# Optimization experiments

Hardware: AMD Instinct MI355X
Metric: run time of the kernel (lower is better)

The kernel has to match this reference:

```python
import jax, jax.numpy as jnp
import numpy as np

N0, N1, N2, N3, B = 120000, 20000, 6000, 1600, 64
E1, E2, E3 = 480000, 144000, 38400
KS = 5  # kernel size per dim; K = 125 total


def spline_basis(pseudo, ks=KS):
    # open B-spline basis, degree 1, over [0,1]^3 (torch_spline_conv semantics)
    p = pseudo * (ks - 1)                       # (E,3)
    lo = jnp.clip(jnp.floor(p), 0.0, ks - 2.0)  # (E,3)
    f = p - lo                                  # fractional part
    bits = jnp.array([[(s >> d) & 1 for d in range(3)] for s in range(8)],
                     dtype=jnp.float32)         # (8,3) corner offsets
    w = jnp.where(bits[None] > 0, f[:, None, :], 1.0 - f[:, None, :])  # (E,8,3)
    basis = w[..., 0] * w[..., 1] * w[..., 2]   # (E,8)
    strides = jnp.array([1.0, ks, ks * ks], dtype=jnp.float32)
    kidx = ((lo[:, None, :] + bits[None]) * strides).sum(-1).astype(jnp.int32)  # (E,8)
    return basis, kidx


def spline_conv(x, edge_index, pseudo, W, root, bias, num_nodes):
    src, dst = edge_index[0], edge_index[1]
    basis, kidx = spline_basis(pseudo)                   # (E,8), (E,8)
    XW = jnp.einsum('ni,kio->nko', x, W)                 # (N,K,out)
    taps = XW[src[:, None], kidx]                        # (E,8,out) gather
    msg = (taps * basis[..., None]).sum(axis=1)          # (E,out)
    agg = jax.ops.segment_sum(msg, dst, num_segments=num_nodes)
    deg = jax.ops.segment_sum(jnp.ones_like(dst, jnp.float32), dst,
                              num_segments=num_nodes)
    agg = agg / jnp.maximum(deg, 1.0)[:, None]           # mean aggregation
    return agg + x @ root + bias


def seg_max(x, seg, n):
    v = jax.ops.segment_max(x, seg, num_segments=n)
    return jnp.where(jnp.isfinite(v), v, 0.0)  # empty voxels -> 0


def setup_inputs() -> dict:
    key = jax.random.key(0)
    ks = jax.random.split(key, 24)
    return {
        'x0': jax.random.uniform(ks[0], (N0, 1), jnp.float32),
        'cluster0': jax.random.randint(ks[1], (N0,), 0, N1),
        'edge1': jax.random.randint(ks[2], (2, E1), 0, N1),
        'pseudo1': jax.random.uniform(ks[3], (E1, 3), jnp.float32),
        'W1': jax.random.normal(ks[4], (125, 1, 64), jnp.float32) * 0.1,
        'root1': jax.random.normal(ks[5], (1, 64), jnp.float32) * 0.1,
        'b1': jnp.zeros((64,), jnp.float32),
        'cluster1': jax.random.randint(ks[6], (N1,), 0, N2),
        'edge2': jax.random.randint(ks[7], (2, E2), 0, N2),
        'pseudo2': jax.random.uniform(ks[8], (E2, 3), jnp.float32),
        'W2': jax.random.normal(ks[9], (125, 64, 64), jnp.float32) * 0.05,
        'root2': jax.random.normal(ks[10], (64, 64), jnp.float32) * 0.05,
        'b2': jnp.zeros((64,), jnp.float32),
        'cluster2': jax.random.randint(ks[11], (N2,), 0, N3),
        'edge3': jax.random.randint(ks[12], (2, E3), 0, N3),
        'pseudo3': jax.random.uniform(ks[13], (E3, 3), jnp.float32),
        'W3': jax.random.normal(ks[14], (125, 64, 128), jnp.float32) * 0.05,
        'root3': jax.random.normal(ks[15], (64, 128), jnp.float32) * 0.05,
        'b3': jnp.zeros((128,), jnp.float32),
        'cluster3': jax.random.randint(ks[16], (N3,), 0, B * 8),
        'fc1_w': jax.random.normal(ks[17], (1024, 256), jnp.float32) * 0.03,
        'fc1_b': jnp.zeros((256,), jnp.float32),
        'fc2_w': jax.random.normal(ks[18], (256, 10), jnp.float32) * 0.06,
        'fc2_b': jnp.zeros((10,), jnp.float32),
    }


def reference(x0, cluster0, edge1, pseudo1, W1, root1, b1,
              cluster1, edge2, pseudo2, W2, root2, b2,
              cluster2, edge3, pseudo3, W3, root3, b3,
              cluster3, fc1_w, fc1_b, fc2_w, fc2_b):
    x = seg_max(x0, cluster0, N1)                       # sparse voxel max pool 1
    x = jax.nn.elu(spline_conv(x, edge1, pseudo1, W1, root1, b1, N1))
    x = seg_max(x, cluster1, N2)                        # pool 2
    x = jax.nn.elu(spline_conv(x, edge2, pseudo2, W2, root2, b2, N2))
    x = seg_max(x, cluster2, N3)                        # pool 3
    x = jax.nn.elu(spline_conv(x, edge3, pseudo3, W3, root3, b3, N3))
    x = seg_max(x, cluster3, B * 8)                     # dense 2x2x2 voxel pool
    x = x.reshape(B, 8 * 128)
    x = jax.nn.elu(x @ fc1_w + fc1_b)
    x = x @ fc2_w + fc2_b
    return jax.nn.log_softmax(x, axis=1)
```

## Files before the change

### kernel.cpp

```cpp
#include <hip/hip_runtime.h>
#include <hip/hip_bf16.h>
#include <math.h>

#define N0c 120000
#define N1c 20000
#define N2c 6000
#define N3c 1600
#define E1c 480000
#define E2c 144000
#define E3c 38400

#define HB1 32
#define HB2 120
#define HB3 40
#define CVT2B 2000
#define CVT3B 4000
#define SS0B  469

typedef __attribute__((ext_vector_type(8))) short short8;
typedef __attribute__((ext_vector_type(4))) float f32x4;

__device__ __forceinline__ float eluf(float x) {
    return x > 0.0f ? x : expm1f(x);
}

__device__ __forceinline__ unsigned f2sort(float f) {
    unsigned u = __float_as_uint(f);
    return (u & 0x80000000u) ? ~u : (u | 0x80000000u);
}
__device__ __forceinline__ float sort2f(unsigned u) {
    unsigned bits = (u & 0x80000000u) ? (u & 0x7FFFFFFFu) : ~u;
    return __uint_as_float(bits);
}
__device__ __forceinline__ unsigned short f2bf(float v) {
    unsigned u = __float_as_uint(v);
    unsigned r = (u + 0x7FFFu + ((u >> 16) & 1u)) >> 16;
    return (unsigned short)r;
}

__global__ __launch_bounds__(256) void hist_all(
    const int* __restrict__ edge1, const int* __restrict__ edge2,
    const int* __restrict__ edge3,
    const float* __restrict__ pseudo2, const float* __restrict__ pseudo3,
    const float* __restrict__ W2, const float* __restrict__ W3,
    const float* __restrict__ x0, const int* __restrict__ cluster0,
    int* __restrict__ blockCnt1,
    int* __restrict__ blockCnt2, int* __restrict__ cntD2,
    int* __restrict__ blockCnt3, int* __restrict__ cntD3,
    unsigned short* __restrict__ W2t, unsigned short* __restrict__ W3t,
    unsigned* __restrict__ xm1)
{
    __shared__ int h[1250];
    int b = blockIdx.x, t = threadIdx.x;
    if (b < HB1) {
        for (int i = t; i < 1250; i += 256) h[i] = 0;
        __syncthreads();
        for (int e = b * 256 + t; e < E1c; e += HB1 * 256)
            atomicAdd(&h[edge1[E1c + e] >> 4], 1);
        __syncthreads();
        for (int i = t; i < 1250; i += 256) blockCnt1[i * HB1 + b] = h[i];
    } else if (b < HB1 + HB2 + HB3) {
        bool is2 = b < HB1 + HB2;
        int rb = is2 ? (b - HB1) : (b - HB1 - HB2);
        int nblk = is2 ? HB2 : HB3;
        int E = is2 ? E2c : E3c;
        const int* edge = is2 ? edge2 : edge3;
        const float* pseudo = is2 ? pseudo2 : pseudo3;
        int* blockCnt = is2 ? blockCnt2 : blockCnt3;
        int* dstCnt = is2 ? cntD2 : cntD3;
        int nb = is2 ? HB2 : HB3;
        if (t < 64) h[t] = 0;
        __syncthreads();
        for (int e = rb * 256 + t; e < E; e += nblk * 256) {
            int c = 0, mul = 1;
            #pragma unroll
            for (int d = 0; d < 3; d++) {
                float p = pseudo[e * 3 + d] * 4.0f;
                float l = fminf(fmaxf(floorf(p), 0.0f), 3.0f);
                c += (int)l * mul;
                mul <<= 2;
            }
            atomicAdd(&h[c], 1);
            atomicAdd(&dstCnt[edge[E + e]], 1);
        }
        __syncthreads();
        if (t < 64) blockCnt[t * nb + rb] = h[t];
    } else if (b < HB1 + HB2 + HB3 + CVT2B) {
        int idx = (b - (HB1 + HB2 + HB3)) * 256 + t;
        if (idx < 125 * 64 * 64) {
            int ic = idx & 63, kn = idx >> 6;
            int n = kn & 63, k = kn >> 6;
            W2t[idx] = f2bf(W2[((size_t)k * 64 + ic) * 64 + n]);
        }
    } else if (b < HB1 + HB2 + HB3 + CVT2B + CVT3B) {
        int idx = (b - (HB1 + HB2 + HB3 + CVT2B)) * 256 + t;
        if (idx < 125 * 128 * 64) {
            int ic = idx & 63, kn = idx >> 6;
            int n = kn & 127, k = kn >> 7;
            W3t[idx] = f2bf(W3[((size_t)k * 64 + ic) * 128 + n]);
        }
    } else {
        int idx = (b - (HB1 + HB2 + HB3 + CVT2B + CVT3B)) * 256 + t;
        if (idx < N0c)
            atomicMax(&xm1[cluster0[idx]], f2sort(x0[idx]));
    }
}

__global__ __launch_bounds__(256) void plan_tot(
    const int* __restrict__ blockCnt1, int* __restrict__ start1,
    const int* __restrict__ blockCnt2, int* __restrict__ binCnt2,
    int* __restrict__ binStart2, int* __restrict__ blkPrefix2,
    int* __restrict__ chunkBin2, int* __restrict__ chunkOff2,
    const int* __restrict__ blockCnt3, int* __restrict__ binCnt3,
    int* __restrict__ binStart3, int* __restrict__ blkPrefix3,
    int* __restrict__ chunkBin3, int* __restrict__ chunkOff3)
{
    __shared__ int ps[256];
    __shared__ int ps64[64];
    int t = threadIdx.x;

    int loc[5];
    int s = 0;
    #pragma unroll
    for (int i = 0; i < 5; i++) {
        int bin = t * 5 + i;
        int v = 0;
        if (bin < 1250) {
            const int4* row = (const int4*)(blockCnt1 + (size_t)bin * HB1);
            #pragma unroll
            for (int j = 0; j < HB1 / 4; j++) {
                int4 q = row[j];
                v += q.x + q.y + q.z + q.w;
            }
        }
        loc[i] = v;
        s += v;
    }
    ps[t] = s;
    __syncthreads();
    for (int ofs = 1; ofs < 256; ofs <<= 1) {
        int add = (t >= ofs) ? ps[t - ofs] : 0;
        __syncthreads();
        ps[t] += add;
        __syncthreads();
    }
    int run = (t == 0) ? 0 : ps[t - 1];
    #pragma unroll
    for (int i = 0; i < 5; i++) {
        int bin = t * 5 + i;
        if (bin < 1250) {
            start1[bin] = run;
            run += loc[i];
        }
    }
    if (t == 255) start1[1250] = run;
    __syncthreads();

    if (t < 64) {
        int v = 0;
        const int4* row = (const int4*)(blockCnt2 + (size_t)t * HB2);
        for (int j = 0; j < HB2 / 4; j++) {
            int4 q = row[j];
            v += q.x + q.y + q.z + q.w;
        }
        binCnt2[t] = v;
        ps64[t] = v;
    }
    __syncthreads();
    if (t == 0) {
        int s2 = 0, p = 0;
        for (int c = 0; c < 64; c++) {
            int v = ps64[c];
            binStart2[c] = s2;
            blkPrefix2[c] = p;
            s2 += v;
            p += (v + 63) >> 6;
        }
        binStart2[64] = s2;
        blkPrefix2[64] = p;
    }
    __syncthreads();
    if (t < 64) {
        int nch = (binCnt2[t] + 63) >> 6;
        int base = blkPrefix2[t];
        for (int j = 0; j < nch; j++) {
            chunkBin2[base + j] = t;
            chunkOff2[base + j] = j;
        }
    }
    __syncthreads();

    if (t < 64) {
        int v = 0;
        const int4* row = (const int4*)(blockCnt3 + (size_t)t * HB3);
        for (int j = 0; j < HB3 / 4; j++) {
            int4 q = row[j];
            v += q.x + q.y + q.z + q.w;
        }
        binCnt3[t] = v;
        ps64[t] = v;
    }
    __syncthreads();
    if (t == 0) {
        int s3 = 0, p = 0;
        for (int c = 0; c < 64; c++) {
            int v = ps64[c];
            binStart3[c] = s3;
            blkPrefix3[c] = p;
            s3 += v;
            p += (v + 63) >> 6;
        }
        binStart3[64] = s3;
        blkPrefix3[64] = p;
    }
    __syncthreads();
    if (t < 64) {
        int nch = (binCnt3[t] + 63) >> 6;
        int base = blkPrefix3[t];
        for (int j = 0; j < nch; j++) {
            chunkBin3[base + j] = t;
            chunkOff3[base + j] = j;
        }
    }
}

__global__ __launch_bounds__(256) void off_all(
    const int* __restrict__ blockCnt1, const int* __restrict__ start1,
    int* __restrict__ blockOff1,
    const int* __restrict__ blockCnt2, const int* __restrict__ binStart2,
    int* __restrict__ blockOff2,
    const int* __restrict__ blockCnt3, const int* __restrict__ binStart3,
    int* __restrict__ blockOff3)
{
    int r = blockIdx.x * 256 + threadIdx.x;
    if (r < 1250) {
        int run = start1[r];
        const int* c = blockCnt1 + (size_t)r * HB1;
        int* o = blockOff1 + (size_t)r * HB1;
        #pragma unroll 4
        for (int b = 0; b < HB1; b++) { o[b] = run; run += c[b]; }
    } else if (r < 1250 + 64) {
        int bin = r - 1250;
        int run = binStart2[bin];
        const int* c = blockCnt2 + (size_t)bin * HB2;
        int* o = blockOff2 + (size_t)bin * HB2;
        #pragma unroll 4
        for (int b = 0; b < HB2; b++) { o[b] = run; run += c[b]; }
    } else if (r < 1250 + 128) {
        int bin = r - 1314;
        int run = binStart3[bin];
        const int* c = blockCnt3 + (size_t)bin * HB3;
        int* o = blockOff3 + (size_t)bin * HB3;
        #pragma unroll 4
        for (int b = 0; b < HB3; b++) { o[b] = run; run += c[b]; }
    }
}

__global__ __launch_bounds__(256) void scatter_all(
    const int* __restrict__ edge1, const float* __restrict__ pseudo1,
    const int* __restrict__ edge2, const float* __restrict__ pseudo2,
    const int* __restrict__ edge3, const float* __restrict__ pseudo3,
    const int* __restrict__ blockOff1, const int* __restrict__ blockOff2,
    const int* __restrict__ blockOff3,
    int4* __restrict__ rec1, int4* __restrict__ rec2, int4* __restrict__ rec3,
    unsigned* __restrict__ xm1)
{
    __shared__ int cur[1250];
    int b = blockIdx.x, t = threadIdx.x;
    if (b < HB1) {
        for (int i = t; i < 1250; i += 256) cur[i] = blockOff1[(size_t)i * HB1 + b];
        __syncthreads();
        for (int e = b * 256 + t; e < E1c; e += HB1 * 256) {
            int src = edge1[e], dst = edge1[E1c + e];
            float f[3];
            int kbase = 0, mul5 = 1;
            #pragma unroll
            for (int d = 0; d < 3; d++) {
                float pp = pseudo1[e * 3 + d] * 4.0f;
                float l = fminf(fmaxf(floorf(pp), 0.0f), 3.0f);
                f[d] = pp - l;
                kbase += (int)l * mul5;
                mul5 *= 5;
            }
            int p = atomicAdd(&cur[dst >> 4], 1);
            rec1[p] = make_int4(src | ((dst & 15) << 16) | (kbase << 20),
                                __float_as_int(f[0]), __float_as_int(f[1]),
                                __float_as_int(f[2]));
        }
    } else if (b < HB1 + HB2 + HB3) {
        bool is2 = b < HB1 + HB2;
        int rb = is2 ? (b - HB1) : (b - HB1 - HB2);
        int nblk = is2 ? HB2 : HB3;
        int E = is2 ? E2c : E3c;
        const int* edge = is2 ? edge2 : edge3;
        const float* pseudo = is2 ? pseudo2 : pseudo3;
        const int* blockOff = is2 ? blockOff2 : blockOff3;
        int4* rec = is2 ? rec2 : rec3;
        int nb = is2 ? HB2 : HB3;
        if (t < 64) cur[t] = blockOff[(size_t)t * nb + rb];
        __syncthreads();
        for (int e = rb * 256 + t; e < E; e += nblk * 256) {
            int src = edge[e], dst = edge[E + e];
            float f[3];
            int c = 0, mul = 1;
            #pragma unroll
            for (int d = 0; d < 3; d++) {
                float pp = pseudo[e * 3 + d] * 4.0f;
                float l = fminf(fmaxf(floorf(pp), 0.0f), 3.0f);
                f[d] = pp - l;
                c += (int)l * mul;
                mul <<= 2;
            }
            int p = atomicAdd(&cur[c], 1);
            rec[p] = make_int4(src | (dst << 16),
                               __float_as_int(f[0]), __float_as_int(f[1]),
                               __float_as_int(f[2]));
        }
    } else {
        int idx = (b - (HB1 + HB2 + HB3)) * 256 + t;
        if (idx < N1c) {
            float f = sort2f(xm1[idx]);
            unsigned bb = __float_as_uint(f);
            if ((bb & 0x7F800000u) == 0x7F800000u) f = 0.0f;
            ((float*)xm1)[idx] = f;
        }
    }
}

__global__ __launch_bounds__(256) void conv1_block(
    const int4* __restrict__ rec, const float* __restrict__ x,
    const int* __restrict__ start,
    const float* __restrict__ W, const float* __restrict__ root,
    const float* __restrict__ bias, const int* __restrict__ cl,
    unsigned* __restrict__ xmOut) {
    __shared__ float T[16][128];
    __shared__ int degL[16];
    int b = blockIdx.x;
    for (int j = threadIdx.x; j < 2048; j += 256) ((float*)T)[j] = 0.0f;
    if (threadIdx.x < 16) degL[threadIdx.x] = 0;
    __syncthreads();
    int s0 = start[b], s1 = start[b + 1];
    for (int i = s0 + threadIdx.x; i < s1; i += 256) {
        int4 r = rec[i];
        int src = r.x & 0xFFFF;
        int ln = (r.x >> 16) & 15;
        int kbase = r.x >> 20;
        float f0 = __int_as_float(r.y);
        float f1 = __int_as_float(r.z);
        float f2 = __int_as_float(r.w);
        float xv = x[src];
        #pragma unroll
        for (int s = 0; s < 8; s++) {
            int b0 = s & 1, b1 = (s >> 1) & 1, b2 = (s >> 2) & 1;
            float w0 = b0 ? f0 : 1.0f - f0;
            float w1 = b1 ? f1 : 1.0f - f1;
            float w2 = b2 ? f2 : 1.0f - f2;
            int k = kbase + b0 + 5 * b1 + 25 * b2;
            atomicAdd(&T[ln][k], xv * w0 * w1 * w2);
        }
        atomicAdd(&degL[ln], 1);
    }
    __syncthreads();
    int w = threadIdx.x >> 6, lane = threadIdx.x & 63;
    float acc[4] = {0.0f, 0.0f, 0.0f, 0.0f};
    for (int k = 0; k < 125; k++) {
        float wv = W[(k << 6) + lane];
        #pragma unroll
        for (int j = 0; j < 4; j++)
            acc[j] = fmaf(T[w + 4 * j][k], wv, acc[j]);
    }
    int v0 = b << 4;
    #pragma unroll
    for (int j = 0; j < 4; j++) {
        int ln = w + 4 * j;
        int v = v0 + ln;
        float d = fmaxf((float)degL[ln], 1.0f);
        float val = eluf(acc[j] / d + x[v] * root[lane] + bias[lane]);
        atomicMax(&xmOut[((size_t)cl[v] << 6) + lane], f2sort(val));
    }
}

__global__ void decode_cvt(unsigned* __restrict__ buf,
                           unsigned short* __restrict__ xb, int total) {
    int idx = blockIdx.x * blockDim.x + threadIdx.x;
    if (idx >= total) return;
    float f = sort2f(buf[idx]);
    unsigned b = __float_as_uint(f);
    if ((b & 0x7F800000u) == 0x7F800000u) f = 0.0f;
    ((float*)buf)[idx] = f;
    xb[idx] = f2bf(f);
}

__global__ void segmax_decode(unsigned* __restrict__ buf, int total) {
    int idx = blockIdx.x * blockDim.x + threadIdx.x;
    if (idx >= total) return;
    float f = sort2f(buf[idx]);
    unsigned b = __float_as_uint(f);
    if ((b & 0x7F800000u) == 0x7F800000u) f = 0.0f;
    ((float*)buf)[idx] = f;
}

template<int COUT>
__global__ __launch_bounds__(256) void spline_mfma(
    const int4* __restrict__ recs,
    const unsigned short* __restrict__ Wt,
    const unsigned short* __restrict__ xb,
    const int* __restrict__ binStart,
    const int* __restrict__ binCnt,
    const int* __restrict__ blkPrefix,
    const int* __restrict__ chunkBin,
    const int* __restrict__ chunkOff,
    float* __restrict__ agg)
{
    __shared__ float basisS[4][8][64];
    __shared__ int srcS[4][64];
    __shared__ int dstS[4][64];

    int w = threadIdx.x >> 6, lane = threadIdx.x & 63;
    int c = blockIdx.x * 4 + w;
    if (c >= blkPrefix[64]) return;
    int bin = chunkBin[c];
    int chunk = chunkOff[c];
    int cnt = binCnt[bin];

    {
        int pos = chunk * 64 + lane;
        bool act = pos < cnt;
        int4 r = act ? recs[binStart[bin] + pos] : make_int4(0, 0, 0, 0);
        srcS[w][lane] = r.x & 0xFFFF;
        dstS[w][lane] = act ? (r.x >> 16) : -1;
        float f0 = __int_as_float(r.y);
        float f1 = __int_as_float(r.z);
        float f2 = __int_as_float(r.w);
        #pragma unroll
        for (int s = 0; s < 8; s++) {
            float w0 = (s & 1) ? f0 : 1.0f - f0;
            float w1 = (s & 2) ? f1 : 1.0f - f1;
            float w2 = (s & 4) ? f2 : 1.0f - f2;
            basisS[w][s][lane] = act ? (w0 * w1 * w2) : 0.0f;
        }
    }
    __builtin_amdgcn_wave_barrier();
    __threadfence_block();

    int lo0 = bin & 3, lo1 = (bin >> 2) & 3, lo2 = bin >> 4;
    int kbase = lo0 + 5 * lo1 + 25 * lo2;
    int colOff = (COUT == 128) ? (blockIdx.y << 6) : 0;
    int q = lane >> 4;
    int mcol = lane & 15;

    short8 afr[4][2];
    #pragma unroll
    for (int rt = 0; rt < 4; rt++) {
        int src = srcS[w][rt * 16 + mcol];
        const unsigned short* xr = xb + ((size_t)src << 6) + q * 8;
        afr[rt][0] = *(const short8*)(xr);
        afr[rt][1] = *(const short8*)(xr + 32);
    }

    f32x4 acc[4][4];
    #pragma unroll
    for (int rt = 0; rt < 4; rt++)
        #pragma unroll
        for (int nt = 0; nt < 4; nt++)
            acc[rt][nt] = (f32x4){0.0f, 0.0f, 0.0f, 0.0f};
    const f32x4 zero4 = {0.0f, 0.0f, 0.0f, 0.0f};

    #pragma unroll 1
    for (int s = 0; s < 8; s++) {
        int k = kbase + (s & 1) + 5 * ((s >> 1) & 1) + 25 * (s >> 2);
        const unsigned short* Wk = Wt + ((size_t)k * COUT + colOff) * 64;
        short8 bfr[4][2];
        #pragma unroll
        for (int nt = 0; nt < 4; nt++) {
            const unsigned short* Wn = Wk + (size_t)(nt * 16 + mcol) * 64 + q * 8;
            bfr[nt][0] = *(const short8*)(Wn);
            bfr[nt][1] = *(const short8*)(Wn + 32);
        }
        #pragma unroll
        for (int rt = 0; rt < 4; rt++) {
            f32x4 ct[4];
            #pragma unroll
            for (int nt = 0; nt < 4; nt++) {
                ct[nt] = __builtin_amdgcn_mfma_f32_16x16x32_bf16(afr[rt][0], bfr[nt][0], zero4, 0, 0, 0);
                ct[nt] = __builtin_amdgcn_mfma_f32_16x16x32_bf16(afr[rt][1], bfr[nt][1], ct[nt], 0, 0, 0);
            }
            #pragma unroll
            for (int r = 0; r < 4; r++) {
                float bs = basisS[w][s][rt * 16 + q * 4 + r];
                #pragma unroll
                for (int nt = 0; nt < 4; nt++)
                    acc[rt][nt][r] = fmaf(bs, ct[nt][r], acc[rt][nt][r]);
            }
        }
    }

    #pragma unroll
    for (int rt = 0; rt < 4; rt++) {
        #pragma unroll
        for (int r = 0; r < 4; r++) {
            int d = dstS[w][rt * 16 + q * 4 + r];
            if (d >= 0) {
                float* ap = agg + (size_t)d * COUT + colOff + mcol;
                #pragma unroll
                for (int nt = 0; nt < 4; nt++)
                    atomicAdd(ap + nt * 16, acc[rt][nt][r]);
            }
        }
    }
}

__global__ __launch_bounds__(256) void node_update64(
    const float* __restrict__ agg, const int* __restrict__ deg,
    const float* __restrict__ xm, const float* __restrict__ root,
    const float* __restrict__ bias, const int* __restrict__ cl,
    unsigned* __restrict__ xmOut, int nNodes) {
    __shared__ float xsh[4][64];
    int w = threadIdx.x >> 6, lane = threadIdx.x & 63;
    int v = blockIdx.x * 4 + w;
    if (v >= nNodes) return;
    xsh[w][lane] = xm[((size_t)v << 6) + lane];
    float a = agg[((size_t)v << 6) + lane] / fmaxf((float)deg[v], 1.0f);
    float r = 0.0f;
    #pragma unroll 8
    for (int i = 0; i < 64; i++)
        r = fmaf(xsh[w][i], root[(i << 6) + lane], r);
    float val = eluf(a + r + bias[lane]);
    atomicMax(&xmOut[((size_t)cl[v] << 6) + lane], f2sort(val));
}

__global__ __launch_bounds__(256) void node_update128(
    const float* __restrict__ agg, const int* __restrict__ deg,
    const float* __restrict__ xm, const float* __restrict__ root,
    const float* __restrict__ bias, const int* __restrict__ cl,
    unsigned* __restrict__ xmOut, int nNodes) {
    __shared__ float xsh[4][64];
    int w = threadIdx.x >> 6, lane = threadIdx.x & 63;
    int v = blockIdx.x * 4 + w;
    if (v >= nNodes) return;
    xsh[w][lane] = xm[((size_t)v << 6) + lane];
    float dinv = 1.0f / fmaxf((float)deg[v], 1.0f);
    float a0 = agg[((size_t)v << 7) + lane] * dinv;
    float a1 = agg[((size_t)v << 7) + 64 + lane] * dinv;
    float r0 = 0.0f, r1 = 0.0f;
    #pragma unroll 8
    for (int i = 0; i < 64; i++) {
        float xi = xsh[w][i];
        r0 = fmaf(xi, root[(i << 7) + lane], r0);
        r1 = fmaf(xi, root[(i << 7) + 64 + lane], r1);
    }
    unsigned* orow = xmOut + ((size_t)cl[v] << 7);
    atomicMax(&orow[lane], f2sort(eluf(a0 + r0 + bias[lane])));
    atomicMax(&orow[64 + lane], f2sort(eluf(a1 + r1 + bias[lane + 64])));
}

__global__ __launch_bounds__(256) void fc1_split(
    const float* __restrict__ xin, const float* __restrict__ w1,
    float* __restrict__ h) {
    __shared__ float xsh[128];
    int row = blockIdx.x, ks = blockIdx.y;
    int o = threadIdx.x;
    if (o < 128) xsh[o] = xin[row * 1024 + ks * 128 + o];
    __syncthreads();
    float acc = 0.0f;
    const float* wp = w1 + (size_t)ks * 128 * 256 + o;
    #pragma unroll 8
    for (int i = 0; i < 128; i++)
        acc = fmaf(xsh[i], wp[i * 256], acc);
    atomicAdd(&h[row * 256 + o], acc);
}

__global__ __launch_bounds__(64) void fc2_k(
    const float* __restrict__ h, const float* __restrict__ b1,
    const float* __restrict__ w2, const float* __restrict__ b2,
    float* __restrict__ out) {
    __shared__ float hs[256];
    __shared__ float lg[10];
    int row = blockIdx.x;
    int t = threadIdx.x;
    for (int i = t; i < 256; i += 64) hs[i] = eluf(h[row * 256 + i] + b1[i]);
    __syncthreads();
    if (t < 10) {
        float a = b2[t];
        for (int i = 0; i < 256; i++) a = fmaf(hs[i], w2[i * 10 + t], a);
        lg[t] = a;
    }
    __syncthreads();
    if (t < 10) {
        float m = -1e30f;
        #pragma unroll
        for (int j = 0; j < 10; j++) m = fmaxf(m, lg[j]);
        float sum = 0.0f;
        #pragma unroll
        for (int j = 0; j < 10; j++) sum += expf(lg[j] - m);
        out[row * 10 + t] = lg[t] - m - logf(sum);
    }
}

extern "C" void kernel_launch(void* const* d_in, const int* in_sizes, int n_in,
                              void* d_out, int out_size, void* d_ws, size_t ws_size,
                              hipStream_t stream) {
    const float* x0      = (const float*)d_in[0];
    const int*   cluster0= (const int*)d_in[1];
    const int*   edge1   = (const int*)d_in[2];
    const float* pseudo1 = (const float*)d_in[3];
    const float* W1      = (const float*)d_in[4];
    const float* root1   = (const float*)d_in[5];
    const float* b1      = (const float*)d_in[6];
    const int*   cluster1= (const int*)d_in[7];
    const int*   edge2   = (const int*)d_in[8];
    const float* pseudo2 = (const float*)d_in[9];
    const float* W2      = (const float*)d_in[10];
    const float* root2   = (const float*)d_in[11];
    const float* b2      = (const float*)d_in[12];
    const int*   cluster2= (const int*)d_in[13];
    const int*   edge3   = (const int*)d_in[14];
    const float* pseudo3 = (const float*)d_in[15];
    const float* W3      = (const float*)d_in[16];
    const float* root3   = (const float*)d_in[17];
    const float* b3      = (const float*)d_in[18];
    const int*   cluster3= (const int*)d_in[19];
    const float* fc1_w   = (const float*)d_in[20];
    const float* fc1_b   = (const float*)d_in[21];
    const float* fc2_w   = (const float*)d_in[22];
    const float* fc2_b   = (const float*)d_in[23];
    float* out = (float*)d_out;

    float* ws = (float*)d_ws;
    size_t off = 0;
    float* xm1  = ws + off; off += 20480;
    float* xm2  = ws + off; off += (size_t)N2c * 64;
    float* xm3  = ws + off; off += (size_t)N3c * 64;
    float* xm4  = ws + off; off += 512 * 128;
    float* agg2 = ws + off; off += (size_t)N2c * 64;
    float* agg3 = ws + off; off += (size_t)N3c * 128;
    float* h1   = ws + off; off += 64 * 256;
    int* cntD2   = (int*)(ws + off); off += 6016;
    int* cntD3   = (int*)(ws + off); off += 1664;
    size_t zeroFloats = off;
    int4* rec1 = (int4*)(ws + off); off += (size_t)E1c * 4;
    int4* rec2 = (int4*)(ws + off); off += (size_t)E2c * 4;
    int4* rec3 = (int4*)(ws + off); off += (size_t)E3c * 4;
    unsigned short* W2t = (unsigned short*)(ws + off); off += 256000;
    unsigned short* W3t = (unsigned short*)(ws + off); off += 512000;
    unsigned short* xb2 = (unsigned short*)(ws + off); off += 192000;
    unsigned short* xb3 = (unsigned short*)(ws + off); off += 51200;
    int* start1    = (int*)(ws + off); off += 1280;
    int* blockCnt1 = (int*)(ws + off); off += HB1 * 1250;
    int* blockOff1 = (int*)(ws + off); off += HB1 * 1250;
    int* blockCnt2 = (int*)(ws + off); off += HB2 * 64;
    int* blockOff2 = (int*)(ws + off); off += HB2 * 64;
    int* blockCnt3 = (int*)(ws + off); off += HB3 * 64;
    int* blockOff3 = (int*)(ws + off); off += HB3 * 64;
    int* binCnt2   = (int*)(ws + off); off += 64;
    int* binStart2 = (int*)(ws + off); off += 80;
    int* blkPrefix2= (int*)(ws + off); off += 80;
    int* chunkBin2 = (int*)(ws + off); off += 2560;
    int* chunkOff2 = (int*)(ws + off); off += 2560;
    int* binCnt3   = (int*)(ws + off); off += 64;
    int* binStart3 = (int*)(ws + off); off += 80;
    int* blkPrefix3= (int*)(ws + off); off += 80;
    int* chunkBin3 = (int*)(ws + off); off += 768;
    int* chunkOff3 = (int*)(ws + off); off += 768;

    hipMemsetAsync(d_ws, 0, zeroFloats * sizeof(float), stream);

    hist_all<<<HB1 + HB2 + HB3 + CVT2B + CVT3B + SS0B, 256, 0, stream>>>(
        edge1, edge2, edge3, pseudo2, pseudo3, W2, W3, x0, cluster0,
        blockCnt1, blockCnt2, cntD2, blockCnt3, cntD3,
        W2t, W3t, (unsigned*)xm1);

    plan_tot<<<1, 256, 0, stream>>>(
        blockCnt1, start1,
        blockCnt2, binCnt2, binStart2, blkPrefix2, chunkBin2, chunkOff2,
        blockCnt3, binCnt3, binStart3, blkPrefix3, chunkBin3, chunkOff3);

    off_all<<<6, 256, 0, stream>>>(
        blockCnt1, start1, blockOff1,
        blockCnt2, binStart2, blockOff2,
        blockCnt3, binStart3, blockOff3);

    scatter_all<<<HB1 + HB2 + HB3 + (N1c + 255) / 256, 256, 0, stream>>>(
        edge1, pseudo1, edge2, pseudo2, edge3, pseudo3,
        blockOff1, blockOff2, blockOff3, rec1, rec2, rec3, (unsigned*)xm1);

    conv1_block<<<1250, 256, 0, stream>>>(rec1, xm1, start1, W1, root1, b1,
                                          cluster1, (unsigned*)xm2);
    decode_cvt<<<(N2c * 64) / 256, 256, 0, stream>>>((unsigned*)xm2, xb2, N2c * 64);

    spline_mfma<64><<<dim3((E2c / 64 + 64 + 3) / 4, 1), 256, 0, stream>>>(
        rec2, W2t, xb2, binStart2, binCnt2, blkPrefix2, chunkBin2, chunkOff2, agg2);
    node_update64<<<(N2c + 3) / 4, 256, 0, stream>>>(agg2, cntD2, xm2, root2, b2,
                                                     cluster2, (unsigned*)xm3, N2c);
    decode_cvt<<<(N3c * 64) / 256, 256, 0, stream>>>((unsigned*)xm3, xb3, N3c * 64);

    spline_mfma<128><<<dim3((E3c / 64 + 64 + 3) / 4, 2), 256, 0, stream>>>(
        rec3, W3t, xb3, binStart3, binCnt3, blkPrefix3, chunkBin3, chunkOff3, agg3);
    node_update128<<<(N3c + 3) / 4, 256, 0, stream>>>(agg3, cntD3, xm3, root3, b3,
                                                      cluster3, (unsigned*)xm4, N3c);
    segmax_decode<<<(512 * 128) / 256, 256, 0, stream>>>((unsigned*)xm4, 512 * 128);

    fc1_split<<<dim3(64, 8), 256, 0, stream>>>(xm4, fc1_w, h1);
    fc2_k<<<64, 64, 0, stream>>>(h1, fc1_b, fc2_w, fc2_b, out);
}
```

Before: 347.4 us.

## Tile weight transpose via LDS, fuse planning kernels, split MFMA columns wider

Weight transpose-and-convert now works one kernel tap per block through a padded LDS tile, giving coalesced reads and packed bf16 pair writes, with far fewer blocks. The offset kernel is merged into the single-block planning kernel, and the segmax decode is folded into fc1's input load, which removes two launches. The spline MFMA kernel now covers 32 output columns per block instead of 64, doubling grid.y for more parallelism and fewer accumulator registers. In exchange, the A fragments and basis are loaded again for each column slice, and more atomic traffic goes to the aggregation buffer.

```diff
diff --git a/kernel.cpp b/kernel.cpp
--- a/kernel.cpp
+++ b/kernel.cpp
@@ -13,9 +13,9 @@
 #define HB1 32
 #define HB2 120
 #define HB3 40
-#define CVT2B 2000
-#define CVT3B 4000
-#define SS0B  469
+#define WT2B 125
+#define WT3B 250
+#define SS0B 469
 
 typedef __attribute__((ext_vector_type(8))) short short8;
 typedef __attribute__((ext_vector_type(4))) float f32x4;
@@ -50,9 +50,10 @@
     unsigned short* __restrict__ W2t, unsigned short* __restrict__ W3t,
     unsigned* __restrict__ xm1)
 {
-    __shared__ int h[1250];
+    __shared__ float tile[64][65];
     int b = blockIdx.x, t = threadIdx.x;
     if (b < HB1) {
+        int* h = (int*)tile;
         for (int i = t; i < 1250; i += 256) h[i] = 0;
         __syncthreads();
         for (int e = b * 256 + t; e < E1c; e += HB1 * 256)
@@ -60,6 +61,7 @@
         __syncthreads();
         for (int i = t; i < 1250; i += 256) blockCnt1[i * HB1 + b] = h[i];
     } else if (b < HB1 + HB2 + HB3) {
+        int* h = (int*)tile;
         bool is2 = b < HB1 + HB2;
         int rb = is2 ? (b - HB1) : (b - HB1 - HB2);
         int nblk = is2 ? HB2 : HB3;
@@ -68,7 +70,6 @@
         const float* pseudo = is2 ? pseudo2 : pseudo3;
         int* blockCnt = is2 ? blockCnt2 : blockCnt3;
         int* dstCnt = is2 ? cntD2 : cntD3;
-        int nb = is2 ? HB2 : HB3;
         if (t < 64) h[t] = 0;
         __syncthreads();
         for (int e = rb * 256 + t; e < E; e += nblk * 256) {
@@ -84,36 +85,60 @@
             atomicAdd(&dstCnt[edge[E + e]], 1);
         }
         __syncthreads();
-        if (t < 64) blockCnt[t * nb + rb] = h[t];
-    } else if (b < HB1 + HB2 + HB3 + CVT2B) {
-        int idx = (b - (HB1 + HB2 + HB3)) * 256 + t;
-        if (idx < 125 * 64 * 64) {
-            int ic = idx & 63, kn = idx >> 6;
-            int n = kn & 63, k = kn >> 6;
-            W2t[idx] = f2bf(W2[((size_t)k * 64 + ic) * 64 + n]);
-        }
-    } else if (b < HB1 + HB2 + HB3 + CVT2B + CVT3B) {
-        int idx = (b - (HB1 + HB2 + HB3 + CVT2B)) * 256 + t;
-        if (idx < 125 * 128 * 64) {
-            int ic = idx & 63, kn = idx >> 6;
-            int n = kn & 127, k = kn >> 7;
-            W3t[idx] = f2bf(W3[((size_t)k * 64 + ic) * 128 + n]);
+        if (t < 64) blockCnt[t * nblk + rb] = h[t];
+    } else if (b < HB1 + HB2 + HB3 + WT2B) {
+        int k = b - (HB1 + HB2 + HB3);
+        int col = t & 63, rq = t >> 6;
+        #pragma unroll
+        for (int i = 0; i < 16; i++) {
+            int ic = i * 4 + rq;
+            tile[ic][col] = W2[((size_t)k * 64 + ic) * 64 + col];
+        }
+        __syncthreads();
+        int n = t >> 2, icq = (t & 3) * 16;
+        unsigned* dst = (unsigned*)(W2t + ((size_t)k * 64 + n) * 64 + icq);
+        #pragma unroll
+        for (int j = 0; j < 8; j++) {
+            unsigned lo = f2bf(tile[icq + 2 * j][n]);
+            unsigned hi = f2bf(tile[icq + 2 * j + 1][n]);
+            dst[j] = lo | (hi << 16);
+        }
+    } else if (b < HB1 + HB2 + HB3 + WT2B + WT3B) {
+        int b2 = b - (HB1 + HB2 + HB3 + WT2B);
+        int k = b2 >> 1, half = (b2 & 1) * 64;
+        int col = t & 63, rq = t >> 6;
+        #pragma unroll
+        for (int i = 0; i < 16; i++) {
+            int ic = i * 4 + rq;
+            tile[ic][col] = W3[((size_t)k * 64 + ic) * 128 + half + col];
+        }
+        __syncthreads();
+        int n = t >> 2, icq = (t & 3) * 16;
+        unsigned* dst = (unsigned*)(W3t + ((size_t)k * 128 + half + n) * 64 + icq);
+        #pragma unroll
+        for (int j = 0; j < 8; j++) {
+            unsigned lo = f2bf(tile[icq + 2 * j][n]);
+            unsigned hi = f2bf(tile[icq + 2 * j + 1][n]);
+            dst[j] = lo | (hi << 16);
         }
     } else {
-        int idx = (b - (HB1 + HB2 + HB3 + CVT2B + CVT3B)) * 256 + t;
+        int idx = (b - (HB1 + HB2 + HB3 + WT2B + WT3B)) * 256 + t;
         if (idx < N0c)
             atomicMax(&xm1[cluster0[idx]], f2sort(x0[idx]));
     }
 }
 
-__global__ __launch_bounds__(256) void plan_tot(
+__global__ __launch_bounds__(256) void plan_all(
     const int* __restrict__ blockCnt1, int* __restrict__ start1,
+    int* __restrict__ blockOff1,
     const int* __restrict__ blockCnt2, int* __restrict__ binCnt2,
     int* __restrict__ binStart2, int* __restrict__ blkPrefix2,
     int* __restrict__ chunkBin2, int* __restrict__ chunkOff2,
+    int* __restrict__ blockOff2,
     const int* __restrict__ blockCnt3, int* __restrict__ binCnt3,
     int* __restrict__ binStart3, int* __restrict__ blkPrefix3,
-    int* __restrict__ chunkBin3, int* __restrict__ chunkOff3)
+    int* __restrict__ chunkBin3, int* __restrict__ chunkOff3,
+    int* __restrict__ blockOff3)
 {
     __shared__ int ps[256];
     __shared__ int ps64[64];
@@ -222,37 +247,28 @@
             chunkOff3[base + j] = j;
         }
     }
-}
-
-__global__ __launch_bounds__(256) void off_all(
-    const int* __restrict__ blockCnt1, const int* __restrict__ start1,
-    int* __restrict__ blockOff1,
-    const int* __restrict__ blockCnt2, const int* __restrict__ binStart2,
-    int* __restrict__ blockOff2,
-    const int* __restrict__ blockCnt3, const int* __restrict__ binStart3,
-    int* __restrict__ blockOff3)
-{
-    int r = blockIdx.x * 256 + threadIdx.x;
-    if (r < 1250) {
-        int run = start1[r];
+    __syncthreads();
+
+    for (int r = t; r < 1250; r += 256) {
+        int rn = start1[r];
         const int* c = blockCnt1 + (size_t)r * HB1;
         int* o = blockOff1 + (size_t)r * HB1;
         #pragma unroll 4
-        for (int b = 0; b < HB1; b++) { o[b] = run; run += c[b]; }
-    } else if (r < 1250 + 64) {
-        int bin = r - 1250;
-        int run = binStart2[bin];
-        const int* c = blockCnt2 + (size_t)bin * HB2;
-        int* o = blockOff2 + (size_t)bin * HB2;
+        for (int bb = 0; bb < HB1; bb++) { o[bb] = rn; rn += c[bb]; }
+    }
+    if (t < 64) {
+        int rn = binStart2[t];
+        const int* c = blockCnt2 + (size_t)t * HB2;
+        int* o = blockOff2 + (size_t)t * HB2;
         #pragma unroll 4
-        for (int b = 0; b < HB2; b++) { o[b] = run; run += c[b]; }
-    } else if (r < 1250 + 128) {
-        int bin = r - 1314;
-        int run = binStart3[bin];
+        for (int bb = 0; bb < HB2; bb++) { o[bb] = rn; rn += c[bb]; }
+    } else if (t < 128) {
+        int bin = t - 64;
+        int rn = binStart3[bin];
         const int* c = blockCnt3 + (size_t)bin * HB3;
         int* o = blockOff3 + (size_t)bin * HB3;
         #pragma unroll 4
-        for (int b = 0; b < HB3; b++) { o[b] = run; run += c[b]; }
+        for (int bb = 0; bb < HB3; bb++) { o[bb] = rn; rn += c[bb]; }
     }
 }
 
@@ -296,8 +312,7 @@
         const float* pseudo = is2 ? pseudo2 : pseudo3;
         const int* blockOff = is2 ? blockOff2 : blockOff3;
         int4* rec = is2 ? rec2 : rec3;
-        int nb = is2 ? HB2 : HB3;
-        if (t < 64) cur[t] = blockOff[(size_t)t * nb + rb];
+        if (t < 64) cur[t] = blockOff[(size_t)t * nblk + rb];
         __syncthreads();
         for (int e = rb * 256 + t; e < E; e += nblk * 256) {
             int src = edge[e], dst = edge[E + e];
@@ -391,15 +406,6 @@
     xb[idx] = f2bf(f);
 }
 
-__global__ void segmax_decode(unsigned* __restrict__ buf, int total) {
-    int idx = blockIdx.x * blockDim.x + threadIdx.x;
-    if (idx >= total) return;
-    float f = sort2f(buf[idx]);
-    unsigned b = __float_as_uint(f);
-    if ((b & 0x7F800000u) == 0x7F800000u) f = 0.0f;
-    ((float*)buf)[idx] = f;
-}
-
 template<int COUT>
 __global__ __launch_bounds__(256) void spline_mfma(
     const int4* __restrict__ recs,
@@ -445,7 +451,7 @@
 
     int lo0 = bin & 3, lo1 = (bin >> 2) & 3, lo2 = bin >> 4;
     int kbase = lo0 + 5 * lo1 + 25 * lo2;
-    int colOff = (COUT == 128) ? (blockIdx.y << 6) : 0;
+    int colOff = blockIdx.y << 5;
     int q = lane >> 4;
     int mcol = lane & 15;
 
@@ -458,11 +464,11 @@
         afr[rt][1] = *(const short8*)(xr + 32);
     }
 
-    f32x4 acc[4][4];
+    f32x4 acc[4][2];
     #pragma unroll
     for (int rt = 0; rt < 4; rt++)
         #pragma unroll
-        for (int nt = 0; nt < 4; nt++)
+        for (int nt = 0; nt < 2; nt++)
             acc[rt][nt] = (f32x4){0.0f, 0.0f, 0.0f, 0.0f};
     const f32x4 zero4 = {0.0f, 0.0f, 0.0f, 0.0f};
 
@@ -470,18 +476,18 @@
     for (int s = 0; s < 8; s++) {
         int k = kbase + (s & 1) + 5 * ((s >> 1) & 1) + 25 * (s >> 2);
         const unsigned short* Wk = Wt + ((size_t)k * COUT + colOff) * 64;
-        short8 bfr[4][2];
-        #pragma unroll
-        for (int nt = 0; nt < 4; nt++) {
+        short8 bfr[2][2];
+        #pragma unroll
+        for (int nt = 0; nt < 2; nt++) {
             const unsigned short* Wn = Wk + (size_t)(nt * 16 + mcol) * 64 + q * 8;
             bfr[nt][0] = *(const short8*)(Wn);
             bfr[nt][1] = *(const short8*)(Wn + 32);
         }
         #pragma unroll
         for (int rt = 0; rt < 4; rt++) {
-            f32x4 ct[4];
+            f32x4 ct[2];
             #pragma unroll
-            for (int nt = 0; nt < 4; nt++) {
+            for (int nt = 0; nt < 2; nt++) {
                 ct[nt] = __builtin_amdgcn_mfma_f32_16x16x32_bf16(afr[rt][0], bfr[nt][0], zero4, 0, 0, 0);
                 ct[nt] = __builtin_amdgcn_mfma_f32_16x16x32_bf16(afr[rt][1], bfr[nt][1], ct[nt], 0, 0, 0);
             }
@@ -489,7 +495,7 @@
             for (int r = 0; r < 4; r++) {
                 float bs = basisS[w][s][rt * 16 + q * 4 + r];
                 #pragma unroll
-                for (int nt = 0; nt < 4; nt++)
+                for (int nt = 0; nt < 2; nt++)
                     acc[rt][nt][r] = fmaf(bs, ct[nt][r], acc[rt][nt][r]);
             }
         }
@@ -503,7 +509,7 @@
             if (d >= 0) {
                 float* ap = agg + (size_t)d * COUT + colOff + mcol;
                 #pragma unroll
-                for (int nt = 0; nt < 4; nt++)
+                for (int nt = 0; nt < 2; nt++)
                     atomicAdd(ap + nt * 16, acc[rt][nt][r]);
             }
         }
@@ -555,12 +561,17 @@
 }
 
 __global__ __launch_bounds__(256) void fc1_split(
-    const float* __restrict__ xin, const float* __restrict__ w1,
+    const unsigned* __restrict__ xin, const float* __restrict__ w1,
     float* __restrict__ h) {
     __shared__ float xsh[128];
     int row = blockIdx.x, ks = blockIdx.y;
     int o = threadIdx.x;
-    if (o < 128) xsh[o] = xin[row * 1024 + ks * 128 + o];
+    if (o < 128) {
+        float f = sort2f(xin[row * 1024 + ks * 128 + o]);
+        unsigned bb = __float_as_uint(f);
+        if ((bb & 0x7F800000u) == 0x7F800000u) f = 0.0f;
+        xsh[o] = f;
+    }
     __syncthreads();
     float acc = 0.0f;
     const float* wp = w1 + (size_t)ks * 128 * 256 + o;
@@ -665,20 +676,15 @@
 
     hipMemsetAsync(d_ws, 0, zeroFloats * sizeof(float), stream);
 
-    hist_all<<<HB1 + HB2 + HB3 + CVT2B + CVT3B + SS0B, 256, 0, stream>>>(
+    hist_all<<<HB1 + HB2 + HB3 + WT2B + WT3B + SS0B, 256, 0, stream>>>(
         edge1, edge2, edge3, pseudo2, pseudo3, W2, W3, x0, cluster0,
         blockCnt1, blockCnt2, cntD2, blockCnt3, cntD3,
         W2t, W3t, (unsigned*)xm1);
 
-    plan_tot<<<1, 256, 0, stream>>>(
-        blockCnt1, start1,
-        blockCnt2, binCnt2, binStart2, blkPrefix2, chunkBin2, chunkOff2,
-        blockCnt3, binCnt3, binStart3, blkPrefix3, chunkBin3, chunkOff3);
-
-    off_all<<<6, 256, 0, stream>>>(
+    plan_all<<<1, 256, 0, stream>>>(
         blockCnt1, start1, blockOff1,
-        blockCnt2, binStart2, blockOff2,
-        blockCnt3, binStart3, blockOff3);
+        blockCnt2, binCnt2, binStart2, blkPrefix2, chunkBin2, chunkOff2, blockOff2,
+        blockCnt3, binCnt3, binStart3, blkPrefix3, chunkBin3, chunkOff3, blockOff3);
 
     scatter_all<<<HB1 + HB2 + HB3 + (N1c + 255) / 256, 256, 0, stream>>>(
         edge1, pseudo1, edge2, pseudo2, edge3, pseudo3,
@@ -688,18 +694,17 @@
                                           cluster1, (unsigned*)xm2);
     decode_cvt<<<(N2c * 64) / 256, 256, 0, stream>>>((unsigned*)xm2, xb2, N2c * 64);
 
-    spline_mfma<64><<<dim3((E2c / 64 + 64 + 3) / 4, 1), 256, 0, stream>>>(
+    spline_mfma<64><<<dim3((E2c / 64 + 64 + 3) / 4, 2), 256, 0, stream>>>(
         rec2, W2t, xb2, binStart2, binCnt2, blkPrefix2, chunkBin2, chunkOff2, agg2);
     node_update64<<<(N2c + 3) / 4, 256, 0, stream>>>(agg2, cntD2, xm2, root2, b2,
                                                      cluster2, (unsigned*)xm3, N2c);
     decode_cvt<<<(N3c * 64) / 256, 256, 0, stream>>>((unsigned*)xm3, xb3, N3c * 64);
 
-    spline_mfma<128><<<dim3((E3c / 64 + 64 + 3) / 4, 2), 256, 0, stream>>>(
+    spline_mfma<128><<<dim3((E3c / 64 + 64 + 3) / 4, 4), 256, 0, stream>>>(
         rec3, W3t, xb3, binStart3, binCnt3, blkPrefix3, chunkBin3, chunkOff3, agg3);
     node_update128<<<(N3c + 3) / 4, 256, 0, stream>>>(agg3, cntD3, xm3, root3, b3,
                                                       cluster3, (unsigned*)xm4, N3c);
-    segmax_decode<<<(512 * 128) / 256, 256, 0, stream>>>((unsigned*)xm4, 512 * 128);
-
-    fc1_split<<<dim3(64, 8), 256, 0, stream>>>(xm4, fc1_w, h1);
+
+    fc1_split<<<dim3(64, 8), 256, 0, stream>>>((unsigned*)xm4, fc1_w, h1);
     fc2_k<<<64, 64, 0, stream>>>(h1, fc1_b, fc2_w, fc2_b, out);
 }
```

Result: no change. 351.6 us (+1.2%).
